# Performance work log

Hardware: AMD Instinct MI355X
Metric: run time of the kernel (lower is better)

Reference implementation:

```python
import jax, jax.numpy as jnp
import numpy as np

N_ROWS = 200_000   # output dim (len(distances))
N_COLS = 200_000   # input dim
NNZ = N_ROWS * 64  # avg 64 neighbors per unitig


def setup_inputs() -> dict:
    key = jax.random.key(0)
    k1, k2, k3, k4, k5 = jax.random.split(key, 5)
    rows = jnp.sort(jax.random.randint(k1, (NNZ,), 0, N_ROWS))  # COO row ids, sorted
    cols = jax.random.randint(k2, (NNZ,), 0, N_COLS)            # COO col ids
    vals = jax.random.normal(k3, (NNZ,), dtype=jnp.float32)     # sparse weight values
    x = jax.random.normal(k4, (N_COLS, 1), dtype=jnp.float32)   # dense input column vector
    bias = jax.random.normal(k5, (N_ROWS,), dtype=jnp.float32)
    return {"vals": vals, "x": x, "bias": bias, "rows": rows, "cols": cols, "n_rows": N_ROWS}


def reference(vals, x, bias, rows, cols, n_rows):
    # y = sparse.mm(W, x).squeeze(1) + bias, W in COO form (rows, cols, vals)
    gathered = vals * x[cols, 0]                      # [nnz]
    y = jax.ops.segment_sum(gathered, rows, num_segments=n_rows,
                            indices_are_sorted=True)  # [n_rows]
    return y + bias
```

## Files before the change

### kernel.cpp

```cpp
#include <hip/hip_runtime.h>


constexpr int       CHUNK = 8;
constexpr int       BLOCK = 256;
constexpr long long SPAN  = (long long)BLOCK * CHUNK;
constexpr int       RMAX  = 768;

typedef float vfloat4 __attribute__((ext_vector_type(4)));
typedef int   vint4   __attribute__((ext_vector_type(4)));

__global__ void init_y_bias(const float* __restrict__ bias,
                            float* __restrict__ y, int n) {
    int i = blockIdx.x * blockDim.x + threadIdx.x;
    if (i < n) y[i] = bias[i];
}

__device__ __forceinline__ void lds_add(float* p, float v) {
    __hip_atomic_fetch_add(p, v, __ATOMIC_RELAXED, __HIP_MEMORY_SCOPE_WORKGROUP);
}

__global__ __launch_bounds__(BLOCK) void spmv_coo_lds(
        const float* __restrict__ vals,
        const float* __restrict__ x,
        const int*   __restrict__ rows,
        const int*   __restrict__ cols,
        const float* __restrict__ bias,
        float*       __restrict__ y,
        long long nnz) {
    __shared__ float acc[RMAX];
    const int tid = threadIdx.x;
    const long long b0 = (long long)blockIdx.x * SPAN;
    if (b0 >= nnz) return;
    const long long bend = (b0 + SPAN < nnz) ? (b0 + SPAN) : nnz;
    const bool full = (b0 + SPAN) <= nnz;

    float v[CHUNK]; int r[CHUNK]; int c[CHUNK];
    const long long i0 = b0 + (long long)tid * CHUNK;
    if (full) {
        const vfloat4* v4 = reinterpret_cast<const vfloat4*>(vals + i0);
        const vint4*   r4 = reinterpret_cast<const vint4*>(rows + i0);
        const vint4*   c4 = reinterpret_cast<const vint4*>(cols + i0);
        #pragma unroll
        for (int q = 0; q < CHUNK / 4; ++q) {
            vfloat4 vv = __builtin_nontemporal_load(v4 + q);
            vint4   rr = __builtin_nontemporal_load(r4 + q);
            vint4   cc = __builtin_nontemporal_load(c4 + q);
            #pragma unroll
            for (int j = 0; j < 4; ++j) {
                v[4*q+j] = vv[j];
                r[4*q+j] = rr[j];
                c[4*q+j] = cc[j];
            }
        }
    }

    #pragma unroll
    for (int i = tid; i < RMAX; i += BLOCK) acc[i] = 0.f;
    const int r0    = rows[b0];
    const int rl    = rows[bend - 1];
    const int range = rl - r0 + 1;
    __syncthreads();

    if (range <= RMAX) {
        if (full) {
            float g[CHUNK];
            #pragma unroll
            for (int k = 0; k < CHUNK; ++k) g[k] = x[c[k]];

            int   cur = r[0];
            float sum = v[0] * g[0];
            #pragma unroll
            for (int k = 1; k < CHUNK; ++k) {
                if (r[k] != cur) {
                    lds_add(&acc[cur - r0], sum);
                    cur = r[k];
                    sum = 0.f;
                }
                sum += v[k] * g[k];
            }
            lds_add(&acc[cur - r0], sum);
        } else if (i0 < bend) {
            int   cur = rows[i0];
            float sum = 0.f;
            long long kend = (i0 + CHUNK < bend) ? (i0 + CHUNK) : bend;
            for (long long k = i0; k < kend; ++k) {
                int rk = rows[k];
                if (rk != cur) { lds_add(&acc[cur - r0], sum); sum = 0.f; cur = rk; }
                sum += vals[k] * x[cols[k]];
            }
            lds_add(&acc[cur - r0], sum);
        }
        __syncthreads();

        for (int i = tid; i < range; i += BLOCK) {
            int   rr = r0 + i;
            float a  = acc[i];
            if (rr == r0 || rr == rl) {
                if (a != 0.f) atomicAdd(&y[rr], a);
            } else {
                y[rr] = bias[rr] + a;
            }
        }
    } else {
        if (i0 < bend) {
            if (full) {
                float g[CHUNK];
                #pragma unroll
                for (int k = 0; k < CHUNK; ++k) g[k] = x[c[k]];
                int   cur = r[0];
                float sum = v[0] * g[0];
                #pragma unroll
                for (int k = 1; k < CHUNK; ++k) {
                    if (r[k] != cur) { atomicAdd(&y[cur], sum); sum = 0.f; cur = r[k]; }
                    sum += v[k] * g[k];
                }
                atomicAdd(&y[cur], sum);
            } else {
                int   cur = rows[i0];
                float sum = 0.f;
                long long kend = (i0 + CHUNK < bend) ? (i0 + CHUNK) : bend;
                for (long long k = i0; k < kend; ++k) {
                    int rk = rows[k];
                    if (rk != cur) { atomicAdd(&y[cur], sum); sum = 0.f; cur = rk; }
                    sum += vals[k] * x[cols[k]];
                }
                atomicAdd(&y[cur], sum);
            }
        }
    }
}

extern "C" void kernel_launch(void* const* d_in, const int* in_sizes, int n_in,
                              void* d_out, int out_size, void* d_ws, size_t ws_size,
                              hipStream_t stream) {
    const float* vals = (const float*)d_in[0];
    const float* x    = (const float*)d_in[1];
    const float* bias = (const float*)d_in[2];
    const int*   rows = (const int*)d_in[3];
    const int*   cols = (const int*)d_in[4];
    float* y = (float*)d_out;

    const long long nnz = in_sizes[0];
    const int n_rows    = in_sizes[2];

    {
        int threads = 256;
        int blocks  = (n_rows + threads - 1) / threads;
        init_y_bias<<<blocks, threads, 0, stream>>>(bias, y, n_rows);
    }

    {
        long long blocks = (nnz + SPAN - 1) / SPAN;
        spmv_coo_lds<<<(int)blocks, BLOCK, 0, stream>>>(
            vals, x, rows, cols, bias, y, nnz);
    }
}
```

Measured before the change: 207.9 us.

## Issue x gathers before barrier, use LDS-only barrier, and double per-thread chunk

```diff
diff --git a/kernel.cpp b/kernel.cpp
--- a/kernel.cpp
+++ b/kernel.cpp
@@ -1,10 +1,10 @@
 #include <hip/hip_runtime.h>
 
 
-constexpr int       CHUNK = 8;
+constexpr int       CHUNK = 16;
 constexpr int       BLOCK = 256;
 constexpr long long SPAN  = (long long)BLOCK * CHUNK;
-constexpr int       RMAX  = 768;
+constexpr int       RMAX  = 1024;
 
 typedef float vfloat4 __attribute__((ext_vector_type(4)));
 typedef int   vint4   __attribute__((ext_vector_type(4)));
@@ -17,6 +17,13 @@
 
 __device__ __forceinline__ void lds_add(float* p, float v) {
     __hip_atomic_fetch_add(p, v, __ATOMIC_RELAXED, __HIP_MEMORY_SCOPE_WORKGROUP);
+}
+
+__device__ __forceinline__ void barrier_lds_only() {
+    __builtin_amdgcn_sched_barrier(0);
+    asm volatile("s_waitcnt lgkmcnt(0)" ::: "memory");
+    __builtin_amdgcn_s_barrier();
+    __builtin_amdgcn_sched_barrier(0);
 }
 
 __global__ __launch_bounds__(BLOCK) void spmv_coo_lds(
@@ -34,39 +41,50 @@
     const long long bend = (b0 + SPAN < nnz) ? (b0 + SPAN) : nnz;
     const bool full = (b0 + SPAN) <= nnz;
 
-    float v[CHUNK]; int r[CHUNK]; int c[CHUNK];
+    const int r0 = rows[b0];
+    const int rl = rows[bend - 1];
+
+    float v[CHUNK]; int r[CHUNK]; int c[CHUNK]; float g[CHUNK];
     const long long i0 = b0 + (long long)tid * CHUNK;
+
     if (full) {
+        const vint4*   c4 = reinterpret_cast<const vint4*>(cols + i0);
         const vfloat4* v4 = reinterpret_cast<const vfloat4*>(vals + i0);
         const vint4*   r4 = reinterpret_cast<const vint4*>(rows + i0);
-        const vint4*   c4 = reinterpret_cast<const vint4*>(cols + i0);
+        #pragma unroll
+        for (int q = 0; q < CHUNK / 4; ++q) {
+            vint4 cc = __builtin_nontemporal_load(c4 + q);
+            #pragma unroll
+            for (int j = 0; j < 4; ++j) c[4*q+j] = cc[j];
+        }
         #pragma unroll
         for (int q = 0; q < CHUNK / 4; ++q) {
             vfloat4 vv = __builtin_nontemporal_load(v4 + q);
-            vint4   rr = __builtin_nontemporal_load(r4 + q);
-            vint4   cc = __builtin_nontemporal_load(c4 + q);
             #pragma unroll
-            for (int j = 0; j < 4; ++j) {
-                v[4*q+j] = vv[j];
-                r[4*q+j] = rr[j];
-                c[4*q+j] = cc[j];
-            }
+            for (int j = 0; j < 4; ++j) v[4*q+j] = vv[j];
+        }
+        #pragma unroll
+        for (int q = 0; q < CHUNK / 4; ++q) {
+            vint4 rr = __builtin_nontemporal_load(r4 + q);
+            #pragma unroll
+            for (int j = 0; j < 4; ++j) r[4*q+j] = rr[j];
         }
     }
 
     #pragma unroll
     for (int i = tid; i < RMAX; i += BLOCK) acc[i] = 0.f;
-    const int r0    = rows[b0];
-    const int rl    = rows[bend - 1];
+
+    if (full) {
+        #pragma unroll
+        for (int k = 0; k < CHUNK; ++k) g[k] = x[c[k]];
+    }
+
     const int range = rl - r0 + 1;
-    __syncthreads();
+
+    barrier_lds_only();
 
     if (range <= RMAX) {
         if (full) {
-            float g[CHUNK];
-            #pragma unroll
-            for (int k = 0; k < CHUNK; ++k) g[k] = x[c[k]];
-
             int   cur = r[0];
             float sum = v[0] * g[0];
             #pragma unroll
@@ -90,7 +108,8 @@
             }
             lds_add(&acc[cur - r0], sum);
         }
-        __syncthreads();
+
+        barrier_lds_only();
 
         for (int i = tid; i < range; i += BLOCK) {
             int   rr = r0 + i;
@@ -104,9 +123,6 @@
     } else {
         if (i0 < bend) {
             if (full) {
-                float g[CHUNK];
-                #pragma unroll
-                for (int k = 0; k < CHUNK; ++k) g[k] = x[c[k]];
                 int   cur = r[0];
                 float sum = v[0] * g[0];
                 #pragma unroll
```

Result: slower. 218.8 us (+5.2%).

## Convert SpMV to persistent grid-stride blocks with software-prefetched next span

Applied to the files above, without the earlier changes.

```diff
diff --git a/kernel.cpp b/kernel.cpp
--- a/kernel.cpp
+++ b/kernel.cpp
@@ -5,6 +5,7 @@
 constexpr int       BLOCK = 256;
 constexpr long long SPAN  = (long long)BLOCK * CHUNK;
 constexpr int       RMAX  = 768;
+constexpr int       GRID_CAP = 2048;
 
 typedef float vfloat4 __attribute__((ext_vector_type(4)));
 typedef int   vint4   __attribute__((ext_vector_type(4)));
@@ -17,6 +18,30 @@
 
 __device__ __forceinline__ void lds_add(float* p, float v) {
     __hip_atomic_fetch_add(p, v, __ATOMIC_RELAXED, __HIP_MEMORY_SCOPE_WORKGROUP);
+}
+
+__device__ __forceinline__ void barrier_lds_only() {
+    asm volatile("s_waitcnt lgkmcnt(0)" ::: "memory");
+    __builtin_amdgcn_s_barrier();
+}
+
+__device__ __forceinline__ void load_span_stream(
+        const float* __restrict__ vals, const int* __restrict__ rows,
+        const int* __restrict__ cols, long long i0,
+        float v[CHUNK], int r[CHUNK], int c[CHUNK]) {
+    const vint4*   c4 = reinterpret_cast<const vint4*>(cols + i0);
+    const vfloat4* v4 = reinterpret_cast<const vfloat4*>(vals + i0);
+    const vint4*   r4 = reinterpret_cast<const vint4*>(rows + i0);
+    #pragma unroll
+    for (int q = 0; q < CHUNK / 4; ++q) {
+        vint4   cc = __builtin_nontemporal_load(c4 + q);
+        vfloat4 vv = __builtin_nontemporal_load(v4 + q);
+        vint4   rr = __builtin_nontemporal_load(r4 + q);
+        #pragma unroll
+        for (int j = 0; j < 4; ++j) {
+            c[4*q+j] = cc[j]; v[4*q+j] = vv[j]; r[4*q+j] = rr[j];
+        }
+    }
 }
 
 __global__ __launch_bounds__(BLOCK) void spmv_coo_lds(
@@ -27,106 +52,128 @@
         const float* __restrict__ bias,
         float*       __restrict__ y,
         long long nnz) {
-    __shared__ float acc[RMAX];
+    __shared__ float acc[2][RMAX];
     const int tid = threadIdx.x;
-    const long long b0 = (long long)blockIdx.x * SPAN;
-    if (b0 >= nnz) return;
-    const long long bend = (b0 + SPAN < nnz) ? (b0 + SPAN) : nnz;
-    const bool full = (b0 + SPAN) <= nnz;
+    const long long nspans = (nnz + SPAN - 1) / SPAN;
+    long long s = blockIdx.x;
+    if (s >= nspans) return;
+    const long long G = gridDim.x;
 
     float v[CHUNK]; int r[CHUNK]; int c[CHUNK];
-    const long long i0 = b0 + (long long)tid * CHUNK;
-    if (full) {
-        const vfloat4* v4 = reinterpret_cast<const vfloat4*>(vals + i0);
-        const vint4*   r4 = reinterpret_cast<const vint4*>(rows + i0);
-        const vint4*   c4 = reinterpret_cast<const vint4*>(cols + i0);
-        #pragma unroll
-        for (int q = 0; q < CHUNK / 4; ++q) {
-            vfloat4 vv = __builtin_nontemporal_load(v4 + q);
-            vint4   rr = __builtin_nontemporal_load(r4 + q);
-            vint4   cc = __builtin_nontemporal_load(c4 + q);
-            #pragma unroll
-            for (int j = 0; j < 4; ++j) {
-                v[4*q+j] = vv[j];
-                r[4*q+j] = rr[j];
-                c[4*q+j] = cc[j];
-            }
-        }
-    }
-
+    float vn[CHUNK]; int rn[CHUNK]; int cn[CHUNK];
+
+    long long b0   = s * SPAN;
+    long long bend = (b0 + SPAN < nnz) ? (b0 + SPAN) : nnz;
+    bool      full = (b0 + SPAN) <= nnz;
+    if (full) load_span_stream(vals, rows, cols, b0 + (long long)tid * CHUNK,
+                               v, r, c);
+    int r0 = rows[b0];
+    int rl = rows[bend - 1];
     #pragma unroll
-    for (int i = tid; i < RMAX; i += BLOCK) acc[i] = 0.f;
-    const int r0    = rows[b0];
-    const int rl    = rows[bend - 1];
-    const int range = rl - r0 + 1;
-    __syncthreads();
-
-    if (range <= RMAX) {
+    for (int i = tid; i < RMAX; i += BLOCK) acc[0][i] = 0.f;
+    int range = rl - r0 + 1;
+    int p = 0;
+    barrier_lds_only();
+
+    while (true) {
+        const long long i0 = b0 + (long long)tid * CHUNK;
+        const long long snext = s + G;
+        const bool have_next = snext < nspans;
+
+        float g[CHUNK];
         if (full) {
-            float g[CHUNK];
             #pragma unroll
             for (int k = 0; k < CHUNK; ++k) g[k] = x[c[k]];
-
-            int   cur = r[0];
-            float sum = v[0] * g[0];
-            #pragma unroll
-            for (int k = 1; k < CHUNK; ++k) {
-                if (r[k] != cur) {
-                    lds_add(&acc[cur - r0], sum);
-                    cur = r[k];
-                    sum = 0.f;
-                }
-                sum += v[k] * g[k];
-            }
-            lds_add(&acc[cur - r0], sum);
-        } else if (i0 < bend) {
-            int   cur = rows[i0];
-            float sum = 0.f;
-            long long kend = (i0 + CHUNK < bend) ? (i0 + CHUNK) : bend;
-            for (long long k = i0; k < kend; ++k) {
-                int rk = rows[k];
-                if (rk != cur) { lds_add(&acc[cur - r0], sum); sum = 0.f; cur = rk; }
-                sum += vals[k] * x[cols[k]];
-            }
-            lds_add(&acc[cur - r0], sum);
-        }
-        __syncthreads();
-
-        for (int i = tid; i < range; i += BLOCK) {
-            int   rr = r0 + i;
-            float a  = acc[i];
-            if (rr == r0 || rr == rl) {
-                if (a != 0.f) atomicAdd(&y[rr], a);
-            } else {
-                y[rr] = bias[rr] + a;
-            }
-        }
-    } else {
-        if (i0 < bend) {
+        }
+
+        long long nb0 = 0, nbend = 0;
+        bool nfull = false;
+        int r0n = 0, rln = 0;
+        if (have_next) {
+            nb0   = snext * SPAN;
+            nbend = (nb0 + SPAN < nnz) ? (nb0 + SPAN) : nnz;
+            nfull = (nb0 + SPAN) <= nnz;
+            if (nfull) load_span_stream(vals, rows, cols,
+                                        nb0 + (long long)tid * CHUNK,
+                                        vn, rn, cn);
+            r0n = rows[nb0];
+            rln = rows[nbend - 1];
+        }
+
+        if (range <= RMAX) {
             if (full) {
-                float g[CHUNK];
-                #pragma unroll
-                for (int k = 0; k < CHUNK; ++k) g[k] = x[c[k]];
                 int   cur = r[0];
                 float sum = v[0] * g[0];
                 #pragma unroll
                 for (int k = 1; k < CHUNK; ++k) {
-                    if (r[k] != cur) { atomicAdd(&y[cur], sum); sum = 0.f; cur = r[k]; }
+                    if (r[k] != cur) {
+                        lds_add(&acc[p][cur - r0], sum);
+                        cur = r[k];
+                        sum = 0.f;
+                    }
                     sum += v[k] * g[k];
                 }
-                atomicAdd(&y[cur], sum);
-            } else {
+                lds_add(&acc[p][cur - r0], sum);
+            } else if (i0 < bend) {
                 int   cur = rows[i0];
                 float sum = 0.f;
                 long long kend = (i0 + CHUNK < bend) ? (i0 + CHUNK) : bend;
                 for (long long k = i0; k < kend; ++k) {
                     int rk = rows[k];
-                    if (rk != cur) { atomicAdd(&y[cur], sum); sum = 0.f; cur = rk; }
+                    if (rk != cur) { lds_add(&acc[p][cur - r0], sum); sum = 0.f; cur = rk; }
                     sum += vals[k] * x[cols[k]];
                 }
-                atomicAdd(&y[cur], sum);
+                lds_add(&acc[p][cur - r0], sum);
             }
-        }
+        } else {
+            if (i0 < bend) {
+                if (full) {
+                    int   cur = r[0];
+                    float sum = v[0] * g[0];
+                    #pragma unroll
+                    for (int k = 1; k < CHUNK; ++k) {
+                        if (r[k] != cur) { atomicAdd(&y[cur], sum); sum = 0.f; cur = r[k]; }
+                        sum += v[k] * g[k];
+                    }
+                    atomicAdd(&y[cur], sum);
+                } else {
+                    int   cur = rows[i0];
+                    float sum = 0.f;
+                    long long kend = (i0 + CHUNK < bend) ? (i0 + CHUNK) : bend;
+                    for (long long k = i0; k < kend; ++k) {
+                        int rk = rows[k];
+                        if (rk != cur) { atomicAdd(&y[cur], sum); sum = 0.f; cur = rk; }
+                        sum += vals[k] * x[cols[k]];
+                    }
+                    atomicAdd(&y[cur], sum);
+                }
+            }
+        }
+        barrier_lds_only();
+
+        if (range <= RMAX) {
+            for (int i = tid; i < range; i += BLOCK) {
+                int   rr = r0 + i;
+                float a  = acc[p][i];
+                if (rr == r0 || rr == rl) {
+                    if (a != 0.f) atomicAdd(&y[rr], a);
+                } else {
+                    y[rr] = bias[rr] + a;
+                }
+            }
+        }
+
+        if (!have_next) break;
+
+        int rangen = rln - r0n + 1;
+        int zrn = (rangen < RMAX) ? rangen : RMAX;
+        for (int i = tid; i < zrn; i += BLOCK) acc[p ^ 1][i] = 0.f;
+        barrier_lds_only();
+
+        s = snext; b0 = nb0; bend = nbend; full = nfull;
+        r0 = r0n; rl = rln; range = rangen; p ^= 1;
+        #pragma unroll
+        for (int k = 0; k < CHUNK; ++k) { v[k] = vn[k]; r[k] = rn[k]; c[k] = cn[k]; }
     }
 }
 
@@ -150,7 +197,8 @@
     }
 
     {
-        long long blocks = (nnz + SPAN - 1) / SPAN;
+        long long nspans = (nnz + SPAN - 1) / SPAN;
+        long long blocks = (nspans < (long long)GRID_CAP) ? nspans : (long long)GRID_CAP;
         spmv_coo_lds<<<(int)blocks, BLOCK, 0, stream>>>(
             vals, x, rows, cols, bias, y, nnz);
     }
```

Result: slower. 219.0 us (+5.4%).
